# Optimization experiments

Measured on AMD Instinct MI355X. Metric: run time of the kernel, lower is better.

Reference implementation:

```python
import jax, jax.numpy as jnp
import numpy as np

B, F, H, W = 2, 8, 16, 16
S = F * H * W                 # 2048 tokens
DIM, NH = 2048, 16
HD = DIM // NH                # 128
C = HD // 2                   # 64 complex pairs per head
CT = C - 2 * (C // 3)         # 22 temporal freqs
CH = C // 3                   # 21 height / 21 width freqs
L = 1024                      # freq table length
SHIFT = 4                     # TCROPE_SHIFT
EPS = 1e-6


def setup_inputs():
    key = jax.random.key(0)
    ks = jax.random.split(key, 12)
    lin = lambda k: jax.random.normal(k, (DIM, DIM), jnp.float32) / np.sqrt(DIM)
    x = jax.random.normal(ks[0], (B, S, DIM), jnp.float32)
    q_w, k_w, v_w, o_w = lin(ks[1]), lin(ks[2]), lin(ks[3]), lin(ks[4])
    q_b = jax.random.normal(ks[5], (DIM,), jnp.float32) * 0.02
    k_b = jax.random.normal(ks[6], (DIM,), jnp.float32) * 0.02
    v_b = jax.random.normal(ks[7], (DIM,), jnp.float32) * 0.02
    o_b = jax.random.normal(ks[8], (DIM,), jnp.float32) * 0.02
    norm_q_w = jnp.ones((DIM,), jnp.float32)
    norm_k_w = jnp.ones((DIM,), jnp.float32)
    # unit-magnitude complex rotations stored as (cos, sin): [L, C, 2]
    inv = 1.0 / (10000.0 ** (np.arange(C, dtype=np.float32) / C))
    ang = np.arange(L, dtype=np.float32)[:, None] * inv[None, :]
    freqs = jnp.asarray(np.stack([np.cos(ang), np.sin(ang)], axis=-1))
    seq_lens = jnp.full((B,), S, jnp.int32)
    grid_sizes = jnp.tile(jnp.array([[F, H, W]], jnp.int32), (B, 1))
    inner_t = jnp.array([[4, 4], [3, 5]], jnp.int32)  # per-sample shot lengths, sum == F
    return dict(x=x, q_w=q_w, q_b=q_b, k_w=k_w, k_b=k_b, v_w=v_w, v_b=v_b,
                o_w=o_w, o_b=o_b, norm_q_w=norm_q_w, norm_k_w=norm_k_w,
                freqs=freqs, seq_lens=seq_lens, grid_sizes=grid_sizes, inner_t=inner_t)


def _rmsnorm(x, w):
    return x * jax.lax.rsqrt(jnp.mean(x * x, axis=-1, keepdims=True) + EPS) * w


def _rope(x, freqs, inner_t, seq_lens):
    # x: [B,S,NH,HD]; per-sample 3D RoPE over (f,h,w) with per-shot temporal index shift.
    xr = x.reshape(B, S, NH, C, 2)
    f0, f1, f2 = freqs[:, :CT], freqs[:, CT:CT + CH], freqs[:, CT + CH:]
    t = jnp.arange(F)
    # frame t belongs to shot j  =>  temporal freq index = j*SHIFT + t  (matches freq_select)
    shot = jax.vmap(lambda it: jnp.searchsorted(jnp.cumsum(it), t, side='right'))(inner_t)
    t_idx = shot * SHIFT + t[None, :]                                   # [B,F]
    tf = jnp.broadcast_to(f0[t_idx][:, :, None, None], (B, F, H, W, CT, 2))
    hf = jnp.broadcast_to(f1[:H][None, None, :, None], (B, F, H, W, CH, 2))
    wf = jnp.broadcast_to(f2[:W][None, None, None, :], (B, F, H, W, CH, 2))
    fr = jnp.concatenate([tf, hf, wf], axis=-2).reshape(B, S, 1, C, 2)  # [B,S,1,C,2]
    a, b = xr[..., 0], xr[..., 1]
    cr, ci = fr[..., 0], fr[..., 1]
    rot = jnp.stack([a * cr - b * ci, a * ci + b * cr], axis=-1).reshape(B, S, NH, HD)
    # positions past f*h*w are left un-rotated in the original (tail concat)
    keep = (jnp.arange(S)[None, :] < seq_lens[:, None])[:, :, None, None]
    return jnp.where(keep, rot, x)


def reference(x, q_w, q_b, k_w, k_b, v_w, v_b, o_w, o_b,
              norm_q_w, norm_k_w, freqs, seq_lens, grid_sizes, inner_t):
    # grid_sizes is (F,H,W) for every sample; baked in as static constants above.
    q = _rmsnorm(x @ q_w + q_b, norm_q_w).reshape(B, S, NH, HD)
    k = _rmsnorm(x @ k_w + k_b, norm_k_w).reshape(B, S, NH, HD)
    v = (x @ v_w + v_b).reshape(B, S, NH, HD)
    q = _rope(q, freqs, inner_t, seq_lens)
    k = _rope(k, freqs, inner_t, seq_lens)
    scores = jnp.einsum('bqnd,bknd->bnqk', q, k) * (HD ** -0.5)
    kmask = (jnp.arange(S)[None, :] < seq_lens[:, None])[:, None, None, :]
    scores = jnp.where(kmask, scores, -1e30)
    attn = jax.nn.softmax(scores, axis=-1)
    out = jnp.einsum('bnqk,bknd->bqnd', attn, v).reshape(B, S, DIM)
    return out @ o_w + o_b
```

## Files before the change

### kernel.cpp

```cpp
#include <hip/hip_runtime.h>


typedef __attribute__((ext_vector_type(8))) short bf16x8;
typedef __attribute__((ext_vector_type(4))) float f32x4;

__device__ __forceinline__ unsigned short f2bf(float f) {
  unsigned int u = __builtin_bit_cast(unsigned int, f);
  u = (u + 0x7FFFu + ((u >> 16) & 1u)) >> 16;
  return (unsigned short)u;
}
__device__ __forceinline__ float bf2f(unsigned short h) {
  unsigned int u = ((unsigned int)h) << 16;
  return __builtin_bit_cast(float, u);
}

#define GLOAD16(gp, lp)                                                        \
  __builtin_amdgcn_global_load_lds(                                            \
      (__attribute__((address_space(1))) void*)(gp),                           \
      (__attribute__((address_space(3))) void*)(lp), 16, 0, 0)

__global__ __launch_bounds__(256) void k_prep(const float* __restrict__ x,
                                              unsigned short* __restrict__ xb,
                                              const float* __restrict__ qw,
                                              const float* __restrict__ kw,
                                              const float* __restrict__ vw,
                                              const float* __restrict__ ow,
                                              unsigned short* __restrict__ qkT,
                                              unsigned short* __restrict__ vT,
                                              unsigned short* __restrict__ oT) {
  const int bid = blockIdx.x;
  const int tid = threadIdx.x;
  if (bid >= 4096) {
    const int i = (bid - 4096) * 256 + tid;
    const float4* p = (const float4*)x + (size_t)i * 2;
    float4 a = p[0], b = p[1];
    bf16x8 v;
    v[0] = (short)f2bf(a.x); v[1] = (short)f2bf(a.y);
    v[2] = (short)f2bf(a.z); v[3] = (short)f2bf(a.w);
    v[4] = (short)f2bf(b.x); v[5] = (short)f2bf(b.y);
    v[6] = (short)f2bf(b.z); v[7] = (short)f2bf(b.w);
    *(bf16x8*)(xb + (size_t)i * 8) = v;
    return;
  }
  __shared__ float tile[64][65];
  const int mat = bid >> 10, t10 = bid & 1023;
  const float* in = (mat == 0) ? qw : (mat == 1) ? kw : (mat == 2) ? vw : ow;
  unsigned short* out = (mat == 0) ? qkT
                      : (mat == 1) ? (qkT + (size_t)2048 * 2048)
                      : (mat == 2) ? vT : oT;
  const int r0 = (t10 >> 5) * 64, c0 = (t10 & 31) * 64;
#pragma unroll
  for (int i = 0; i < 4; i++) {
    const int fi = tid + i * 256;
    const int row = fi >> 4, c4 = fi & 15;
    float4 v = *(const float4*)(in + (size_t)(r0 + row) * 2048 + c0 + c4 * 4);
    tile[row][c4 * 4 + 0] = v.x; tile[row][c4 * 4 + 1] = v.y;
    tile[row][c4 * 4 + 2] = v.z; tile[row][c4 * 4 + 3] = v.w;
  }
  __syncthreads();
#pragma unroll
  for (int i = 0; i < 2; i++) {
    const int oi = tid + i * 256;
    const int c = oi >> 3, r8 = oi & 7;
    bf16x8 o;
#pragma unroll
    for (int j = 0; j < 8; j++) o[j] = (short)f2bf(tile[r8 * 8 + j][c]);
    *(bf16x8*)(out + (size_t)(c0 + c) * 2048 + r0 + r8 * 8) = o;
  }
}

template <int OUTF32, int BIASMODE>
__global__ __launch_bounds__(256) void k_gemm(const unsigned short* __restrict__ A,
                                              const unsigned short* __restrict__ BT,
                                              void* __restrict__ Cout,
                                              const float* __restrict__ bias,
                                              int M, int N, int K) {
  __shared__ unsigned short As[128 * 32];
  __shared__ unsigned short Bs[128 * 32];
  const int tid = threadIdx.x;
  const int lane = tid & 63, w = tid >> 6;
  const int g = lane >> 4, cc = lane & 15;
  const int gx = gridDim.x;
  int id = blockIdx.y * gx + blockIdx.x;
  const int tot = gx * gridDim.y;
  id = (id & 7) * (tot >> 3) + (id >> 3);
  const int n0 = (id % gx) * 128, m0 = (id / gx) * 128;
  const int wm = (w >> 1) * 64, wn = (w & 1) * 64;
  f32x4 acc[4][4] = {};
  const unsigned short* Ab = A + (size_t)m0 * K;
  const unsigned short* Bb = BT + (size_t)n0 * K;
  const int r0 = tid >> 2, c0 = (tid & 3) * 8;
  for (int kt = 0; kt < K; kt += 32) {
    GLOAD16(Ab + (size_t)r0 * K + kt + c0, As + tid * 8);
    GLOAD16(Ab + (size_t)(r0 + 64) * K + kt + c0, As + (tid + 256) * 8);
    GLOAD16(Bb + (size_t)r0 * K + kt + c0, Bs + tid * 8);
    GLOAD16(Bb + (size_t)(r0 + 64) * K + kt + c0, Bs + (tid + 256) * 8);
    __syncthreads();
    bf16x8 af[4], bfr[4];
#pragma unroll
    for (int m4 = 0; m4 < 4; m4++)
      af[m4] = *(const bf16x8*)(As + (wm + m4 * 16 + cc) * 32 + g * 8);
#pragma unroll
    for (int n4 = 0; n4 < 4; n4++)
      bfr[n4] = *(const bf16x8*)(Bs + (wn + n4 * 16 + cc) * 32 + g * 8);
#pragma unroll
    for (int m4 = 0; m4 < 4; m4++)
#pragma unroll
      for (int n4 = 0; n4 < 4; n4++)
        acc[m4][n4] = __builtin_amdgcn_mfma_f32_16x16x32_bf16(af[m4], bfr[n4],
                                                              acc[m4][n4], 0, 0, 0);
    __syncthreads();
  }
#pragma unroll
  for (int m4 = 0; m4 < 4; m4++)
#pragma unroll
    for (int n4 = 0; n4 < 4; n4++) {
      const int col = n0 + wn + n4 * 16 + cc;
#pragma unroll
      for (int r = 0; r < 4; r++) {
        const int row = m0 + wm + m4 * 16 + g * 4 + r;
        float v = acc[m4][n4][r];
        if (BIASMODE == 1) v += bias[row];
        if (BIASMODE == 2) v += bias[col];
        if (OUTF32)
          ((float*)Cout)[(size_t)row * N + col] = v;
        else
          ((unsigned short*)Cout)[(size_t)row * N + col] = f2bf(v);
      }
    }
}

__device__ __forceinline__ void stage_half(const unsigned short* __restrict__ src,
                                           int K, unsigned short* dst, int tid) {
#pragma unroll
  for (int j = 0; j < 2; j++) {
    const int li = tid + j * 512;
    const int r = li >> 3;
    const int c16 = (li & 7) ^ (r & 7);
    GLOAD16(src + (size_t)r * K + c16 * 8, (char*)dst + li * 16);
  }
}

__global__ __launch_bounds__(512, 2) void k_gemm_yqk(const unsigned short* __restrict__ A,
                                                     const unsigned short* __restrict__ BT,
                                                     unsigned short* __restrict__ Cout) {
  __shared__ unsigned short As[2][256 * 64];
  __shared__ unsigned short Bs[2][256 * 64];
  const int tid = threadIdx.x;
  const int lane = tid & 63, w = tid >> 6;
  const int g = lane >> 4, cc = lane & 15;
  const int wm = (w >> 2) * 128, wn = (w & 3) * 64;
  const int swz = (cc & 7) << 4;
  const int N = 4096, K = 2048;
  int id = blockIdx.x;
  id = (id & 7) * 32 + (id >> 3);
  const int m0 = (id >> 4) * 256, n0 = (id & 15) * 256;
  f32x4 acc[8][4] = {};
  const int T = K >> 6;

  stage_half(BT + (size_t)n0 * K, K, Bs[0], tid);
  stage_half(A + (size_t)m0 * K, K, As[0], tid);
  stage_half(BT + (size_t)(n0 + 128) * K, K, Bs[0] + 8192, tid);
  stage_half(A + (size_t)(m0 + 128) * K, K, As[0] + 8192, tid);
  stage_half(BT + (size_t)n0 * K + 64, K, Bs[1], tid);
  stage_half(A + (size_t)m0 * K + 64, K, As[1], tid);
  asm volatile("s_waitcnt vmcnt(4)" ::: "memory");
  __builtin_amdgcn_s_barrier();

  for (int t = 0; t < T; ++t) {
    const int c = t & 1;
    const char* Ac = (const char*)As[c];
    const char* Bc = (const char*)Bs[c];
    bf16x8 ar[4][2], br[4][2];
#pragma unroll
    for (int m = 0; m < 4; m++)
#pragma unroll
      for (int kk = 0; kk < 2; kk++)
        ar[m][kk] = *(const bf16x8*)(Ac + (wm + m * 16 + cc) * 128 +
                                     ((kk * 64 + g * 16) ^ swz));
#pragma unroll
    for (int n = 0; n < 2; n++)
#pragma unroll
      for (int kk = 0; kk < 2; kk++)
        br[n][kk] = *(const bf16x8*)(Bc + (wn + n * 16 + cc) * 128 +
                                     ((kk * 64 + g * 16) ^ swz));
    stage_half(BT + (size_t)(n0 + 128) * K + ((t + 1) & (T - 1)) * 64, K,
               Bs[c ^ 1] + 8192, tid);
    __builtin_amdgcn_s_barrier();
    asm volatile("s_waitcnt lgkmcnt(0)" ::: "memory");
    __builtin_amdgcn_sched_barrier(0);
    __builtin_amdgcn_s_setprio(1);
#pragma unroll
    for (int kk = 0; kk < 2; kk++)
#pragma unroll
      for (int m = 0; m < 4; m++)
#pragma unroll
        for (int n = 0; n < 2; n++)
          acc[m][n] = __builtin_amdgcn_mfma_f32_16x16x32_bf16(ar[m][kk], br[n][kk],
                                                              acc[m][n], 0, 0, 0);
    __builtin_amdgcn_s_setprio(0);
    __builtin_amdgcn_s_barrier();
#pragma unroll
    for (int n = 2; n < 4; n++)
#pragma unroll
      for (int kk = 0; kk < 2; kk++)
        br[n][kk] = *(const bf16x8*)(Bc + (wn + n * 16 + cc) * 128 +
                                     ((kk * 64 + g * 16) ^ swz));
    stage_half(A + (size_t)(m0 + 128) * K + ((t + 1) & (T - 1)) * 64, K,
               As[c ^ 1] + 8192, tid);
    __builtin_amdgcn_s_barrier();
    asm volatile("s_waitcnt lgkmcnt(0)" ::: "memory");
    __builtin_amdgcn_sched_barrier(0);
    __builtin_amdgcn_s_setprio(1);
#pragma unroll
    for (int kk = 0; kk < 2; kk++)
#pragma unroll
      for (int m = 0; m < 4; m++)
#pragma unroll
        for (int n = 2; n < 4; n++)
          acc[m][n] = __builtin_amdgcn_mfma_f32_16x16x32_bf16(ar[m][kk], br[n][kk],
                                                              acc[m][n], 0, 0, 0);
    __builtin_amdgcn_s_setprio(0);
    __builtin_amdgcn_s_barrier();
#pragma unroll
    for (int m = 0; m < 4; m++)
#pragma unroll
      for (int kk = 0; kk < 2; kk++)
        ar[m][kk] = *(const bf16x8*)(Ac + (wm + (m + 4) * 16 + cc) * 128 +
                                     ((kk * 64 + g * 16) ^ swz));
    stage_half(BT + (size_t)n0 * K + ((t + 2) & (T - 1)) * 64, K, Bs[c], tid);
    __builtin_amdgcn_s_barrier();
    asm volatile("s_waitcnt lgkmcnt(0)" ::: "memory");
    __builtin_amdgcn_sched_barrier(0);
    __builtin_amdgcn_s_setprio(1);
#pragma unroll
    for (int kk = 0; kk < 2; kk++)
#pragma unroll
      for (int m = 0; m < 4; m++)
#pragma unroll
        for (int n = 0; n < 2; n++)
          acc[m + 4][n] = __builtin_amdgcn_mfma_f32_16x16x32_bf16(ar[m][kk], br[n][kk],
                                                                  acc[m + 4][n], 0, 0, 0);
    __builtin_amdgcn_s_setprio(0);
    __builtin_amdgcn_s_barrier();
    stage_half(A + (size_t)m0 * K + ((t + 2) & (T - 1)) * 64, K, As[c], tid);
    __builtin_amdgcn_s_setprio(1);
#pragma unroll
    for (int kk = 0; kk < 2; kk++)
#pragma unroll
      for (int m = 0; m < 4; m++)
#pragma unroll
        for (int n = 2; n < 4; n++)
          acc[m + 4][n] = __builtin_amdgcn_mfma_f32_16x16x32_bf16(ar[m][kk], br[n][kk],
                                                                  acc[m + 4][n], 0, 0, 0);
    __builtin_amdgcn_s_setprio(0);
    if (t < T - 2)
      asm volatile("s_waitcnt vmcnt(4)" ::: "memory");
    else
      asm volatile("s_waitcnt vmcnt(0)" ::: "memory");
    __builtin_amdgcn_sched_barrier(0);
    __builtin_amdgcn_s_barrier();
  }

#pragma unroll
  for (int mi = 0; mi < 8; mi++)
#pragma unroll
    for (int n = 0; n < 4; n++) {
      const int col = n0 + wn + n * 16 + cc;
#pragma unroll
      for (int j = 0; j < 4; j++) {
        const int row = m0 + wm + mi * 16 + g * 4 + j;
        Cout[(size_t)row * N + col] = f2bf(acc[mi][n][j]);
      }
    }
}

__global__ __launch_bounds__(256) void k_qk_epi(const unsigned short* __restrict__ Yqk,
                                                const float* __restrict__ q_b,
                                                const float* __restrict__ k_b,
                                                const float* __restrict__ nqw,
                                                const float* __restrict__ nkw,
                                                const float* __restrict__ freqs,
                                                const int* __restrict__ inner_t,
                                                unsigned short* __restrict__ Q,
                                                unsigned short* __restrict__ K) {
  const int row = blockIdx.x;
  const int b = row >> 11, s = row & 2047;
  const int t = threadIdx.x;
  const unsigned short* yr = Yqk + (size_t)row * 4096;
  bf16x8 yq = *(const bf16x8*)(yr + t * 8);
  bf16x8 yk = *(const bf16x8*)(yr + 2048 + t * 8);
  float4 qb0 = *(const float4*)(q_b + t * 8), qb1 = *(const float4*)(q_b + t * 8 + 4);
  float4 kb0 = *(const float4*)(k_b + t * 8), kb1 = *(const float4*)(k_b + t * 8 + 4);
  float q[8], k[8];
  q[0] = bf2f((unsigned short)yq[0]) + qb0.x; q[1] = bf2f((unsigned short)yq[1]) + qb0.y;
  q[2] = bf2f((unsigned short)yq[2]) + qb0.z; q[3] = bf2f((unsigned short)yq[3]) + qb0.w;
  q[4] = bf2f((unsigned short)yq[4]) + qb1.x; q[5] = bf2f((unsigned short)yq[5]) + qb1.y;
  q[6] = bf2f((unsigned short)yq[6]) + qb1.z; q[7] = bf2f((unsigned short)yq[7]) + qb1.w;
  k[0] = bf2f((unsigned short)yk[0]) + kb0.x; k[1] = bf2f((unsigned short)yk[1]) + kb0.y;
  k[2] = bf2f((unsigned short)yk[2]) + kb0.z; k[3] = bf2f((unsigned short)yk[3]) + kb0.w;
  k[4] = bf2f((unsigned short)yk[4]) + kb1.x; k[5] = bf2f((unsigned short)yk[5]) + kb1.y;
  k[6] = bf2f((unsigned short)yk[6]) + kb1.z; k[7] = bf2f((unsigned short)yk[7]) + kb1.w;
  float ssq = 0.f, ssk = 0.f;
#pragma unroll
  for (int j = 0; j < 8; j++) { ssq += q[j] * q[j]; ssk += k[j] * k[j]; }
#pragma unroll
  for (int off = 32; off; off >>= 1) {
    ssq += __shfl_xor(ssq, off);
    ssk += __shfl_xor(ssk, off);
  }
  __shared__ float red[8];
  const int w = t >> 6;
  if ((t & 63) == 0) { red[w] = ssq; red[4 + w] = ssk; }
  __syncthreads();
  const float sq = red[0] + red[1] + red[2] + red[3];
  const float sk = red[4] + red[5] + red[6] + red[7];
  const float rq = __builtin_amdgcn_rsqf(sq * (1.0f / 2048.0f) + 1e-6f);
  const float rk = __builtin_amdgcn_rsqf(sk * (1.0f / 2048.0f) + 1e-6f);
  float4 nq0 = *(const float4*)(nqw + t * 8), nq1 = *(const float4*)(nqw + t * 8 + 4);
  float4 nk0 = *(const float4*)(nkw + t * 8), nk1 = *(const float4*)(nkw + t * 8 + 4);
  q[0] *= rq * nq0.x; q[1] *= rq * nq0.y; q[2] *= rq * nq0.z; q[3] *= rq * nq0.w;
  q[4] *= rq * nq1.x; q[5] *= rq * nq1.y; q[6] *= rq * nq1.z; q[7] *= rq * nq1.w;
  k[0] *= rk * nk0.x; k[1] *= rk * nk0.y; k[2] *= rk * nk0.z; k[3] *= rk * nk0.w;
  k[4] *= rk * nk1.x; k[5] *= rk * nk1.y; k[6] *= rk * nk1.z; k[7] *= rk * nk1.w;
  const int f = s >> 8, hh = (s >> 4) & 15, ww = s & 15;
  const int it0 = inner_t[b * 2], it1 = inner_t[b * 2 + 1];
  const int trow = ((f >= it0) + (f >= it0 + it1)) * 4 + f;
#pragma unroll
  for (int jj = 0; jj < 4; jj++) {
    const int c = (t * 4 + jj) & 63;
    const int fr = (c < 22) ? trow : ((c < 43) ? hh : ww);
    const float cr = freqs[((size_t)fr * 64 + c) * 2];
    const float ci = freqs[((size_t)fr * 64 + c) * 2 + 1];
    float a = q[2 * jj], bb = q[2 * jj + 1];
    q[2 * jj] = a * cr - bb * ci; q[2 * jj + 1] = a * ci + bb * cr;
    a = k[2 * jj]; bb = k[2 * jj + 1];
    k[2 * jj] = a * cr - bb * ci; k[2 * jj + 1] = a * ci + bb * cr;
  }
  const float QSCALE = 0.08838834764831845f * 1.4426950408889634f;
  bf16x8 oq, ok;
#pragma unroll
  for (int j = 0; j < 8; j++) {
    oq[j] = (short)f2bf(q[j] * QSCALE);
    ok[j] = (short)f2bf(k[j]);
  }
  const int head = t >> 4, d0 = (t & 15) * 8;
  const size_t off = ((size_t)(b * 16 + head) * 2048 + s) * 128 + d0;
  *(bf16x8*)(Q + off) = oq;
  *(bf16x8*)(K + off) = ok;
}

__global__ __launch_bounds__(512, 4) void k_attn(const unsigned short* __restrict__ Q,
                                                 const unsigned short* __restrict__ K,
                                                 const unsigned short* __restrict__ V,
                                                 unsigned short* __restrict__ O) {
  __shared__ unsigned short Ks[2][64 * 128];
  __shared__ unsigned short Vs[2][128 * 64];
  __shared__ unsigned short Ps[8 * 16 * 64];
  const int tid = threadIdx.x;
  const int lane = tid & 63, w = tid >> 6;
  const int g = lane >> 4, cc = lane & 15;
  const int orig = blockIdx.x;
  const int lid = (orig & 7) * 64 + (orig >> 3);
  const int bh = lid >> 4;
  const int q0 = (lid & 15) * 128;
  const int b = bh >> 4, h = bh & 15;

  const unsigned short* Qb = Q + ((size_t)bh * 2048 + q0 + w * 16 + cc) * 128;
  bf16x8 qf[4];
#pragma unroll
  for (int kk = 0; kk < 4; kk++) qf[kk] = *(const bf16x8*)(Qb + kk * 32 + g * 8);

  const char* kbase = (const char*)(K + (size_t)bh * 2048 * 128);
  const char* vbase = (const char*)V + ((size_t)h * 128 * 4096 + (size_t)b * 2048) * 2;

  f32x4 acc[8] = {};
  float mloc = -3.0e38f, lloc = 0.f;
  char* Pb = (char*)Ps + w * 2048 + cc * 128;
  const int psw = (cc & 7) << 4;
  const int gbase = (lane & 48) | (((lane >> 4) & 3) << 2);
  const f32x4 vzero = {0.f, 0.f, 0.f, 0.f};

#define ATTN_STAGE(s0, bi)                                                     \
  {                                                                            \
    const char* kt0 = kbase + (size_t)(s0) * 256;                              \
    const char* vt0 = vbase + (size_t)(s0) * 2;                                \
    char* Kd = (char*)(Ks[bi]);                                                \
    char* Vd = (char*)(Vs[bi]);                                                \
    _Pragma("unroll") for (int i = 0; i < 2; i++) {                            \
      const int li = i * 512 + tid;                                            \
      const int kr = li >> 4;                                                  \
      const int kc = ((li & 15) * 16) ^ ((kr & 7) << 4);                       \
      GLOAD16(kt0 + kr * 256 + kc, Kd + li * 16);                              \
      const int vd = li >> 3;                                                  \
      const int vc = ((li & 7) * 16) ^ ((vd & 7) << 4);                        \
      GLOAD16(vt0 + (size_t)vd * 8192 + vc, Vd + li * 16);                     \
    }                                                                          \
  }

  ATTN_STAGE(0, 0);
  for (int t = 0; t < 32; ++t) {
    const int cur = t & 1;
    if (t < 31) {
      ATTN_STAGE((t + 1) * 64, cur ^ 1);
      asm volatile("s_waitcnt vmcnt(4)" ::: "memory");
    } else {
      asm volatile("s_waitcnt vmcnt(0)" ::: "memory");
    }
    __builtin_amdgcn_sched_barrier(0);
    __builtin_amdgcn_s_barrier();

    const char* kcur = (const char*)(Ks[cur]);
    const int sw = (cc & 7) << 4;
    f32x4 sf[4] = {vzero, vzero, vzero, vzero};
    __builtin_amdgcn_s_setprio(1);
#pragma unroll
    for (int kk = 0; kk < 4; kk++) {
      const int ko = (kk * 64 + g * 16) ^ sw;
      bf16x8 kf0 = *(const bf16x8*)(kcur + (cc)*256 + ko);
      bf16x8 kf1 = *(const bf16x8*)(kcur + (16 + cc) * 256 + ko);
      bf16x8 kf2 = *(const bf16x8*)(kcur + (32 + cc) * 256 + ko);
      bf16x8 kf3 = *(const bf16x8*)(kcur + (48 + cc) * 256 + ko);
      sf[0] = __builtin_amdgcn_mfma_f32_16x16x32_bf16(kf0, qf[kk], sf[0], 0, 0, 0);
      sf[1] = __builtin_amdgcn_mfma_f32_16x16x32_bf16(kf1, qf[kk], sf[1], 0, 0, 0);
      sf[2] = __builtin_amdgcn_mfma_f32_16x16x32_bf16(kf2, qf[kk], sf[2], 0, 0, 0);
      sf[3] = __builtin_amdgcn_mfma_f32_16x16x32_bf16(kf3, qf[kk], sf[3], 0, 0, 0);
    }
    __builtin_amdgcn_s_setprio(0);

    float tm = fmaxf(fmaxf(fmaxf(sf[0][0], sf[0][1]), fmaxf(sf[0][2], sf[0][3])),
                     fmaxf(fmaxf(sf[1][0], sf[1][1]), fmaxf(sf[1][2], sf[1][3])));
    tm = fmaxf(tm, fmaxf(fmaxf(fmaxf(sf[2][0], sf[2][1]), fmaxf(sf[2][2], sf[2][3])),
                         fmaxf(fmaxf(sf[3][0], sf[3][1]), fmaxf(sf[3][2], sf[3][3]))));
    tm = fmaxf(tm, __shfl_xor(tm, 16));
    tm = fmaxf(tm, __shfl_xor(tm, 32));
    if (__any(tm > mloc + 8.0f)) {
      const float mn = fmaxf(mloc, tm);
      const float sc = __builtin_amdgcn_exp2f(mloc - mn);
      mloc = mn;
      lloc *= sc;
      f32x4 scv;
#pragma unroll
      for (int r = 0; r < 4; r++) scv[r] = __shfl(sc, gbase + r);
#pragma unroll
      for (int d4 = 0; d4 < 8; d4++) acc[d4] *= scv;
    }
    float rs = 0.f;
#pragma unroll
    for (int n4 = 0; n4 < 4; n4++) {
      const float p0 = __builtin_amdgcn_exp2f(sf[n4][0] - mloc);
      const float p1 = __builtin_amdgcn_exp2f(sf[n4][1] - mloc);
      const float p2 = __builtin_amdgcn_exp2f(sf[n4][2] - mloc);
      const float p3 = __builtin_amdgcn_exp2f(sf[n4][3] - mloc);
      rs += (p0 + p1) + (p2 + p3);
      unsigned lo, hi;
      asm("v_cvt_pk_bf16_f32 %0, %1, %2" : "=v"(lo) : "v"(p0), "v"(p1));
      asm("v_cvt_pk_bf16_f32 %0, %1, %2" : "=v"(hi) : "v"(p2), "v"(p3));
      uint2 pv_; pv_.x = lo; pv_.y = hi;
      *(uint2*)(Pb + ((n4 * 32 + g * 8) ^ psw)) = pv_;
    }
    rs += __shfl_xor(rs, 16);
    rs += __shfl_xor(rs, 32);
    lloc += rs;

    const char* vcur = (const char*)(Vs[cur]);
    __builtin_amdgcn_s_setprio(1);
#pragma unroll
    for (int ks = 0; ks < 2; ks++) {
      bf16x8 pf = *(const bf16x8*)(Pb + ((ks * 64 + g * 16) ^ psw));
#pragma unroll
      for (int d4 = 0; d4 < 8; d4++) {
        const int dd = d4 * 16 + cc;
        bf16x8 vf = *(const bf16x8*)(vcur + dd * 128 +
                                     ((ks * 64 + g * 16) ^ ((dd & 7) << 4)));
        acc[d4] = __builtin_amdgcn_mfma_f32_16x16x32_bf16(pf, vf, acc[d4], 0, 0, 0);
      }
    }
    __builtin_amdgcn_s_setprio(0);

    asm volatile("s_waitcnt lgkmcnt(0)" ::: "memory");
    __builtin_amdgcn_sched_barrier(0);
    __builtin_amdgcn_s_barrier();
  }
#undef ATTN_STAGE

  const float invl = __builtin_amdgcn_rcpf(lloc);
  float ir[4];
#pragma unroll
  for (int r = 0; r < 4; r++) ir[r] = __shfl(invl, gbase + r);
  unsigned short* Ob = O + (size_t)(b * 2048 + q0 + w * 16) * 2048 + h * 128;
#pragma unroll
  for (int d4 = 0; d4 < 8; d4++)
#pragma unroll
    for (int r = 0; r < 4; r++)
      Ob[(size_t)(g * 4 + r) * 2048 + d4 * 16 + cc] = f2bf(acc[d4][r] * ir[r]);
}

extern "C" void kernel_launch(void* const* d_in, const int* in_sizes, int n_in,
                              void* d_out, int out_size, void* d_ws, size_t ws_size,
                              hipStream_t stream) {
  const float* x     = (const float*)d_in[0];
  const float* q_w   = (const float*)d_in[1];
  const float* q_b   = (const float*)d_in[2];
  const float* k_w   = (const float*)d_in[3];
  const float* k_b   = (const float*)d_in[4];
  const float* v_w   = (const float*)d_in[5];
  const float* v_b   = (const float*)d_in[6];
  const float* o_w   = (const float*)d_in[7];
  const float* o_b   = (const float*)d_in[8];
  const float* nqw   = (const float*)d_in[9];
  const float* nkw   = (const float*)d_in[10];
  const float* freqs = (const float*)d_in[11];
  const int* inner_t = (const int*)d_in[14];

  const size_t NEED = (size_t)112 << 20;
  if (ws_size < NEED) return;

  char* ws = (char*)d_ws;
  unsigned short* xb   = (unsigned short*)(ws);
  unsigned short* WqkT = (unsigned short*)(ws + ((size_t)16 << 20));
  unsigned short* WvT  = (unsigned short*)(ws + ((size_t)32 << 20));
  unsigned short* WoT  = (unsigned short*)(ws + ((size_t)40 << 20));
  unsigned short* Yqk  = (unsigned short*)(ws + ((size_t)48 << 20));
  unsigned short* Vt   = (unsigned short*)(ws + ((size_t)80 << 20));
  unsigned short* Kr   = (unsigned short*)(ws + ((size_t)96 << 20));
  unsigned short* Qr   = xb;
  unsigned short* Orow = WqkT;

  k_prep<<<8192, 256, 0, stream>>>(x, xb, q_w, k_w, v_w, o_w, WqkT, WvT, WoT);
  k_gemm_yqk<<<256, 512, 0, stream>>>(xb, WqkT, Yqk);
  k_gemm<0, 1><<<dim3(32, 16), 256, 0, stream>>>(WvT, xb, Vt, v_b, 2048, 4096, 2048);
  k_qk_epi<<<4096, 256, 0, stream>>>(Yqk, q_b, k_b, nqw, nkw, freqs, inner_t, Qr, Kr);
  k_attn<<<512, 512, 0, stream>>>(Qr, Kr, Vt, Orow);
  k_gemm<1, 2><<<dim3(16, 32), 256, 0, stream>>>(Orow, WoT, (float*)d_out, o_b, 4096, 2048, 2048);
}
```

Measured before the change: 313.6 us.

## Fuse V projection into the QK GEMM launch with shared 256x256 tile routine

Factors the 256x256 tiled GEMM body into a device function with an optional bias and runtime M/N/K. It launches one 384-block kernel that computes both the QK projection and the transposed V projection, which replaces the separate generic k_gemm launch for V. The aim is to drop one launch, fill the GPU better with a single larger grid, and run the V GEMM on the tuned pipelined tile path. The cost is a per-element bias branch in the epilogue, and the block-id remap must correctly cover 384 tiles.

After: 357.6 us. +14.0%, slower.

```diff
diff --git a/kernel.cpp b/kernel.cpp
--- a/kernel.cpp
+++ b/kernel.cpp
@@ -141,9 +141,11 @@
   }
 }
 
-__global__ __launch_bounds__(512, 2) void k_gemm_yqk(const unsigned short* __restrict__ A,
-                                                     const unsigned short* __restrict__ BT,
-                                                     unsigned short* __restrict__ Cout) {
+__device__ __forceinline__ void gemm256(const unsigned short* __restrict__ A,
+                                        const unsigned short* __restrict__ BT,
+                                        unsigned short* __restrict__ Cout,
+                                        const float* __restrict__ bias, int biasrow,
+                                        int m0, int n0, int N, int K) {
   __shared__ unsigned short As[2][256 * 64];
   __shared__ unsigned short Bs[2][256 * 64];
   const int tid = threadIdx.x;
@@ -151,10 +153,6 @@
   const int g = lane >> 4, cc = lane & 15;
   const int wm = (w >> 2) * 128, wn = (w & 3) * 64;
   const int swz = (cc & 7) << 4;
-  const int N = 4096, K = 2048;
-  int id = blockIdx.x;
-  id = (id & 7) * 32 + (id >> 3);
-  const int m0 = (id >> 4) * 256, n0 = (id & 15) * 256;
   f32x4 acc[8][4] = {};
   const int T = K >> 6;
 
@@ -270,9 +268,27 @@
 #pragma unroll
       for (int j = 0; j < 4; j++) {
         const int row = m0 + wm + mi * 16 + g * 4 + j;
-        Cout[(size_t)row * N + col] = f2bf(acc[mi][n][j]);
+        float v = acc[mi][n][j];
+        if (bias) v += biasrow ? bias[row] : bias[col];
+        Cout[(size_t)row * N + col] = f2bf(v);
       }
     }
+}
+
+__global__ __launch_bounds__(512, 2) void k_gemm_qkv(const unsigned short* __restrict__ xb,
+                                                     const unsigned short* __restrict__ WqkT,
+                                                     const unsigned short* __restrict__ WvT,
+                                                     unsigned short* __restrict__ Yqk,
+                                                     unsigned short* __restrict__ Vt,
+                                                     const float* __restrict__ v_b) {
+  const int orig = blockIdx.x;
+  int id = (orig & 7) * 48 + (orig >> 3);
+  if (id < 256) {
+    gemm256(xb, WqkT, Yqk, nullptr, 0, (id >> 4) * 256, (id & 15) * 256, 4096, 2048);
+  } else {
+    id -= 256;
+    gemm256(WvT, xb, Vt, v_b, 1, (id >> 4) * 256, (id & 15) * 256, 4096, 2048);
+  }
 }
 
 __global__ __launch_bounds__(256) void k_qk_epi(const unsigned short* __restrict__ Yqk,
@@ -528,8 +544,7 @@
   unsigned short* Orow = WqkT;
 
   k_prep<<<8192, 256, 0, stream>>>(x, xb, q_w, k_w, v_w, o_w, WqkT, WvT, WoT);
-  k_gemm_yqk<<<256, 512, 0, stream>>>(xb, WqkT, Yqk);
-  k_gemm<0, 1><<<dim3(32, 16), 256, 0, stream>>>(WvT, xb, Vt, v_b, 2048, 4096, 2048);
+  k_gemm_qkv<<<384, 512, 0, stream>>>(xb, WqkT, WvT, Yqk, Vt, v_b);
   k_qk_epi<<<4096, 256, 0, stream>>>(Yqk, q_b, k_b, nqw, nkw, freqs, inner_t, Qr, Kr);
   k_attn<<<512, 512, 0, stream>>>(Qr, Kr, Vt, Orow);
   k_gemm<1, 2><<<dim3(16, 32), 256, 0, stream>>>(Orow, WoT, (float*)d_out, o_b, 4096, 2048, 2048);
```
